# Optimization experiments

Hardware: AMD Instinct MI355X
Metric: run time of the kernel (lower is better)

The kernel has to match this reference:

```python
import jax, jax.numpy as jnp
import numpy as np

N = 16384          # nodes
E_R = 524288       # radial edges (avg degree 32)
E_B = 32768        # bonded edges
N_TYPES = 20       # atom types
CS = 64            # scalar (0e) channels
CV = 32            # vector (1o) channels
EA = 16            # edge_attr_dim
EA_B = EA // 2     # bondedness embedding dim
EA_R = (EA + 1) // 2  # radial basis dim
CUTOFF = 1.5       # effective_radial_cutoff
L = 2              # n_layers
NORM = float(np.sqrt((E_R + E_B) / N))  # ~sqrt(avg degree) message normalization


def setup_inputs() -> dict:
    key = jax.random.key(0)
    ks = jax.random.split(key, 32)
    def rn(i, shape, scale=1.0):
        return jax.random.normal(ks[i], shape, dtype=jnp.float32) * scale
    s_e = 1.0 / np.sqrt(EA)
    inp = {}
    inp["pos"] = rn(0, (N, 3))
    inp["c_noise"] = rn(1, (1,))
    inp["atom_types"] = jax.random.randint(ks[2], (N,), 0, N_TYPES)
    inp["radial_edge_index"] = jax.random.randint(ks[3], (2, E_R), 0, N)
    inp["bonded_edge_index"] = jax.random.randint(ks[4], (2, E_B), 0, N)
    # learned parameters
    inp["atom_tab"] = rn(5, (N_TYPES, CS))
    inp["bond_tab"] = rn(6, (2, EA_B))
    inp["ns0_w"] = rn(7, (CS,), 0.1)
    inp["We0"] = rn(8, (EA, CS), s_e)
    inp["We1"] = rn(9, (EA, CS), s_e)
    inp["Wself0"] = rn(10, (CS, CS), 1.0 / np.sqrt(CS))
    inp["Ws0"] = rn(11, (CS, CS), 1.0 / np.sqrt(CS))
    inp["Wv0"] = rn(12, (CS, CV), 1.0 / np.sqrt(CS))
    inp["ns_w"] = rn(13, (L, CS + CV), 0.1)
    inp["We_ss"] = rn(14, (L, EA, CS), s_e)
    inp["We_vs"] = rn(15, (L, EA, CV), s_e)
    inp["We_sv"] = rn(16, (L, EA, CS), s_e)
    inp["We_vv"] = rn(17, (L, EA, CV), s_e)
    inp["We_vx"] = rn(18, (L, EA, CV), s_e)
    inp["Wmix_s"] = rn(19, (L, CS + CV, CS), 1.0 / np.sqrt(CS + CV))
    inp["Wmix_v"] = rn(20, (L, CS + 2 * CV, CV), 1.0 / np.sqrt(CS + 2 * CV))
    inp["Wself_s"] = rn(21, (L, CS, CS), 1.0 / np.sqrt(CS))
    inp["Wself_v"] = rn(22, (L, CV, CV), 1.0 / np.sqrt(CV))
    inp["skip_w"] = rn(23, (L, 2 * (CS + CV)), 0.1)
    inp["skip_b"] = rn(24, (L, 2 * (CS + CV)), 0.1)
    inp["w_out"] = rn(25, (CV,), 1.0 / np.sqrt(CV))
    inp["gain"] = jnp.asarray(0.5, dtype=jnp.float32)
    return inp


def _radial_basis(d):
    # e3nn soft_one_hot_linspace, basis='gaussian', cutoff=True
    centers = jnp.linspace(0.0, CUTOFF, EA_R + 2)[1:-1]
    step = centers[1] - centers[0]
    diff = (d[:, None] - centers[None, :]) / step
    return jnp.exp(-diff * diff) * 1.12


def reference(pos, c_noise, atom_tab, bond_tab, ns0_w, We0, We1, Wself0, Ws0, Wv0,
              ns_w, We_ss, We_vs, We_sv, We_vv, We_vx, Wmix_s, Wmix_v, Wself_s, Wself_v,
              skip_w, skip_b, w_out, gain, atom_types, radial_edge_index, bonded_edge_index):
    edge_index = jnp.concatenate([radial_edge_index, bonded_edge_index], axis=1)
    bond_mask = jnp.concatenate([jnp.zeros((E_R,), jnp.int32), jnp.ones((E_B,), jnp.int32)])
    src, dst = edge_index[0], edge_index[1]
    edge_vec = pos[src] - pos[dst]                      # [E,3]
    d = jnp.sqrt(jnp.sum(edge_vec * edge_vec, -1) + 1e-12)
    Y1 = jnp.sqrt(3.0) * edge_vec / d[:, None]          # l=1 SH, component norm; Y0 == 1
    edge_attr = jnp.concatenate([bond_tab[bond_mask], _radial_basis(d)], axis=-1)  # [E,EA]

    # atom embedding + initial noise-conditional scaling
    s = atom_tab[atom_types] * (1.0 + c_noise * ns0_w)  # [N,CS]

    # initial projector: scalar-input equivariant conv -> hidden irreps
    w0 = edge_attr @ We0
    w1 = edge_attr @ We1
    s_src = s[src]
    a_s = jax.ops.segment_sum(w0 * s_src, dst, num_segments=N) / NORM
    a_v = jax.ops.segment_sum((w1 * s_src)[:, :, None] * Y1[:, None, :], dst, num_segments=N) / NORM
    s_h = a_s @ Ws0 + s @ Wself0                        # [N,CS]
    v_h = jnp.einsum('nci,cd->ndi', a_v, Wv0)           # [N,CV,3]

    for l in range(L):
        # noise-conditional scaling (per-irrep-channel scalar scale)
        scale = 1.0 + c_noise * ns_w[l]
        ss = s_h * scale[:CS]
        vv = v_h * scale[CS:][None, :, None]
        ss_e = ss[src]
        vv_e = vv[src]
        # edge-attr-conditioned tensor-product weights
        w_ss = edge_attr @ We_ss[l]
        w_vs = edge_attr @ We_vs[l]
        w_sv = edge_attr @ We_sv[l]
        w_vv = edge_attr @ We_vv[l]
        w_vx = edge_attr @ We_vx[l]
        # CG tensor-product messages: 0x0->0, 1x1->0 (dot), 0x1->1, 1x0->1, 1x1->1 (cross)
        vdot = jnp.einsum('eci,ei->ec', vv_e, Y1)
        m_s = jnp.concatenate([w_ss * ss_e, w_vs * vdot], axis=-1)          # [E,CS+CV]
        m_v = jnp.concatenate([
            (w_sv * ss_e)[:, :, None] * Y1[:, None, :],
            w_vv[:, :, None] * vv_e,
            w_vx[:, :, None] * jnp.cross(vv_e, Y1[:, None, :]),
        ], axis=1)                                                          # [E,CS+2CV,3]
        a_s = jax.ops.segment_sum(m_s, dst, num_segments=N) / NORM
        a_v = jax.ops.segment_sum(m_v, dst, num_segments=N) / NORM
        new_s = a_s @ Wmix_s[l] + ss @ Wself_s[l]
        new_v = jnp.einsum('nci,cd->ndi', a_v, Wmix_v[l]) + jnp.einsum('nci,cd->ndi', vv, Wself_v[l])
        # noise-conditional skip connection (gated residual)
        g = jax.nn.sigmoid(skip_b[l] + c_noise * skip_w[l])
        s_h = g[:CS] * s_h + g[CS:2 * CS] * new_s
        g_v = g[2 * CS:]
        v_h = g_v[:CV][None, :, None] * v_h + g_v[CV:][None, :, None] * new_v

    # output head: 1o vectors -> 3D displacement, times output gain
    return jnp.einsum('nci,c->ni', v_h, w_out) * gain
```

## Files before the change

kernel.cpp:

```cpp
#include <hip/hip_runtime.h>
#include <math.h>

#define NA 16384
#define ER 524288
#define EB 32768
#define ET 557056
#define INV_NORM 0.17149858514250882f
#define SQRT3 1.7320508075688772f
#define RB_STEP (1.5f/9.0f)
#define BINS 512
#define DMAX 2.5f
#define INV_H ((float)BINS / DMAX)
#define T0U (2 * BINS * 128)
#define TLU (2 * BINS * 256)

typedef unsigned int uint32;
typedef unsigned short ushort16;
typedef float vf4 __attribute__((ext_vector_type(4)));
typedef float vf2 __attribute__((ext_vector_type(2)));

__device__ __forceinline__ float sigmoidf_(float x) { return 1.f / (1.f + __expf(-x)); }

__device__ __forceinline__ ushort16 f2bf(float x) {
  uint32 u = __float_as_uint(x);
  u = u + 0x7FFFu + ((u >> 16) & 1u);
  return (ushort16)(u >> 16);
}
__device__ __forceinline__ uint32 packbf(float hi, float lo) {
  return ((uint32)f2bf(hi) << 16) | (uint32)f2bf(lo);
}
__device__ __forceinline__ float bfhi(uint32 u) { return __uint_as_float(u & 0xFFFF0000u); }
__device__ __forceinline__ float bflo(uint32 u) { return __uint_as_float(u << 16); }

__device__ __forceinline__ float4 ntl4(const float* p) {
  vf4 v = __builtin_nontemporal_load((const vf4*)p);
  return make_float4(v.x, v.y, v.z, v.w);
}
__device__ __forceinline__ float2 ntl2(const float* p) {
  vf2 v = __builtin_nontemporal_load((const vf2*)p);
  return make_float2(v.x, v.y);
}
__device__ __forceinline__ void nts4(float* p, float a, float b, float c, float d) {
  vf4 v; v.x = a; v.y = b; v.z = c; v.w = d;
  __builtin_nontemporal_store(v, (vf4*)p);
}
__device__ __forceinline__ void nts2(float* p, float a, float b) {
  vf2 v; v.x = a; v.y = b;
  __builtin_nontemporal_store(v, (vf2*)p);
}

__global__ void k_hist(const int* __restrict__ rad, const int* __restrict__ bon, int* __restrict__ count) {
  int e = blockIdx.x * 256 + threadIdx.x;
  int d = (e < ER) ? rad[ER + e] : bon[EB + (e - ER)];
  atomicAdd(&count[d], 1);
}

__global__ void k_scan1(const int* __restrict__ count, int* __restrict__ partial) {
  __shared__ int red[256];
  int b = blockIdx.x, t = threadIdx.x;
  red[t] = count[b * 256 + t];
  __syncthreads();
  for (int s = 128; s > 0; s >>= 1) {
    if (t < s) red[t] += red[t + s];
    __syncthreads();
  }
  if (t == 0) partial[b] = red[0];
}

__global__ void k_scan2(int* __restrict__ partial) {
  int run = 0;
  for (int i = 0; i < 64; ++i) { int c = partial[i]; partial[i] = run; run += c; }
}

__global__ void k_scan3(const int* __restrict__ count, const int* __restrict__ partial,
                        int* __restrict__ offsets, int* __restrict__ cursor) {
  __shared__ int sc[256];
  int b = blockIdx.x, t = threadIdx.x;
  int v = count[b * 256 + t];
  sc[t] = v;
  __syncthreads();
  for (int off = 1; off < 256; off <<= 1) {
    int x = (t >= off) ? sc[t - off] : 0;
    __syncthreads();
    sc[t] += x;
    __syncthreads();
  }
  int excl = sc[t] - v + partial[b];
  offsets[b * 256 + t] = excl;
  cursor[b * 256 + t] = excl;
  if (b == 63 && t == 255) offsets[NA] = excl + v;
}

__global__ void k_fill_embed(const int* __restrict__ rad, const int* __restrict__ bon,
                             int* __restrict__ cursor, int* __restrict__ sorted,
                             const float* __restrict__ atom_tab, const int* __restrict__ types,
                             const float* __restrict__ ns0_w, const float* __restrict__ cnoise,
                             float* __restrict__ s_feat, ushort16* __restrict__ s_bf) {
  if (blockIdx.x < ET / 256) {
    int e = blockIdx.x * 256 + threadIdx.x;
    int d = (e < ER) ? rad[ER + e] : bon[EB + (e - ER)];
    int slot = atomicAdd(&cursor[d], 1);
    sorted[slot] = e;
  } else {
    int tid = (blockIdx.x - ET / 256) * 256 + threadIdx.x;
    int n = tid >> 6, c = tid & 63;
    float cn = cnoise[0];
    float v = atom_tab[types[n] * 64 + c] * (1.f + cn * ns0_w[c]);
    s_feat[tid] = v;
    s_bf[tid] = f2bf(v);
  }
}

__global__ void k_reorder(const int* __restrict__ sorted,
                          const int* __restrict__ rad, const int* __restrict__ bon,
                          const float* __restrict__ pos, float* __restrict__ rec8) {
  int idx = blockIdx.x * 256 + threadIdx.x;
  int e = sorted[idx];
  int src, dst, v;
  if (e < ER) { src = rad[e]; dst = rad[ER + e]; v = 0; }
  else        { src = bon[e - ER]; dst = bon[EB + e - ER]; v = 1; }
  float dx = pos[src * 3] - pos[dst * 3];
  float dy = pos[src * 3 + 1] - pos[dst * 3 + 1];
  float dz = pos[src * 3 + 2] - pos[dst * 3 + 2];
  float dist = sqrtf(dx * dx + dy * dy + dz * dz + 1e-12f);
  float inv = 1.f / dist;
  float fq = fminf(dist * INV_H, BINS - 1.001f);
  int q = (int)fq;
  float frac = fq - (float)q;
  int qoffL = (v * BINS + q) << 8;
  float* rp = rec8 + (size_t)idx * 8;
  nts4(rp, __int_as_float(src), SQRT3 * dx * inv, SQRT3 * dy * inv, SQRT3 * dz * inv);
  nts2(rp + 4, frac, __int_as_float(qoffL));
}

__global__ void k_build(const float* __restrict__ We0, const float* __restrict__ We1,
                        const float* __restrict__ We_ss, const float* __restrict__ We_vs,
                        const float* __restrict__ We_sv, const float* __restrict__ We_vv,
                        const float* __restrict__ We_vx, const float* __restrict__ bond_tab,
                        uint32* __restrict__ T0, uint32* __restrict__ TL) {
  int q = blockIdx.x, t = blockIdx.y, v = blockIdx.z, c = threadIdx.x;
  float d0 = q * (DMAX / BINS), d1 = (q + 1) * (DMAX / BINS);
  float rb0[8], rb1[8];
#pragma unroll
  for (int k = 0; k < 8; ++k) {
    float f0 = (d0 - (k + 1) * RB_STEP) * (1.f / RB_STEP);
    float f1 = (d1 - (k + 1) * RB_STEP) * (1.f / RB_STEP);
    rb0[k] = 1.12f * __expf(-f0 * f0);
    rb1[k] = 1.12f * __expf(-f1 * f1);
  }
  if (t == 0) {
    float ba = 0, bb = 0, a0 = 0, a1 = 0, b0 = 0, b1 = 0;
#pragma unroll
    for (int k = 0; k < 8; ++k) {
      float bt = bond_tab[v * 8 + k];
      float av_lo = We0[k * 64 + c], av_hi = We0[(8 + k) * 64 + c];
      float bv_lo = We1[k * 64 + c], bv_hi = We1[(8 + k) * 64 + c];
      ba += bt * av_lo; bb += bt * bv_lo;
      a0 += rb0[k] * av_hi; a1 += rb1[k] * av_hi;
      b0 += rb0[k] * bv_hi; b1 += rb1[k] * bv_hi;
    }
    uint32* o = T0 + (((size_t)v * BINS + q) << 7) + c * 2;
    o[0] = packbf(ba + a0, a1 - a0);
    o[1] = packbf(bb + b0, b1 - b0);
  } else {
    int l = t - 1;
    const float* Wss = We_ss + l * 1024;
    const float* Wsv = We_sv + l * 1024;
    const float* WA = (c < 32) ? (We_vs + l * 512) : (We_vx + l * 512);
    const float* WB = (c < 32) ? (We_vv + l * 512) : nullptr;
    int cu = c & 31;
    float sa = 0, sb = 0, s0 = 0, s1 = 0, t0 = 0, t1 = 0;
    float ua = 0, ub = 0, u0 = 0, u1 = 0, w0 = 0, w1 = 0;
#pragma unroll
    for (int k = 0; k < 8; ++k) {
      float bt = bond_tab[v * 8 + k];
      float ss_lo = Wss[k * 64 + c], ss_hi = Wss[(8 + k) * 64 + c];
      float sv_lo = Wsv[k * 64 + c], sv_hi = Wsv[(8 + k) * 64 + c];
      sa += bt * ss_lo; sb += bt * sv_lo;
      s0 += rb0[k] * ss_hi; s1 += rb1[k] * ss_hi;
      t0 += rb0[k] * sv_hi; t1 += rb1[k] * sv_hi;
      float a_lo = WA[k * 32 + cu], a_hi = WA[(8 + k) * 32 + cu];
      ua += bt * a_lo;
      u0 += rb0[k] * a_hi; u1 += rb1[k] * a_hi;
      if (WB) {
        float b_lo = WB[k * 32 + cu], b_hi = WB[(8 + k) * 32 + cu];
        ub += bt * b_lo;
        w0 += rb0[k] * b_hi; w1 += rb1[k] * b_hi;
      }
    }
    uint32* o = TL + (size_t)l * TLU + (((size_t)v * BINS + q) << 8) + c * 4;
    o[0] = packbf(sa + s0, s1 - s0);
    o[1] = packbf(sb + t0, t1 - t0);
    o[2] = packbf(ua + u0, u1 - u0);
    o[3] = WB ? packbf(ub + w0, w1 - w0) : 0u;
  }
}

__global__ __launch_bounds__(256, 8) void k_agg0(
    const int* __restrict__ offsets, const float* __restrict__ rec8,
    const uint32* __restrict__ T0, const ushort16* __restrict__ s_bf,
    float* __restrict__ a_s, uint32* __restrict__ a_v) {
  int lane = threadIdx.x & 63;
  int n = blockIdx.x * 4 + (threadIdx.x >> 6);
  float acc = 0, a0 = 0, a1 = 0, a2 = 0;
  int beg = __builtin_amdgcn_readfirstlane(offsets[n]);
  int end = __builtin_amdgcn_readfirstlane(offsets[n + 1]);
  if (beg < end) {
    int last = end - 1;
    int e1 = (beg + 1 < end) ? beg + 1 : last;
    int e2 = (beg + 2 < end) ? beg + 2 : last;
    const float* p0 = rec8 + (size_t)beg * 8;
    const float* p1 = rec8 + (size_t)e1 * 8;
    const float* p2 = rec8 + (size_t)e2 * 8;
    float4 rA0 = ntl4(p0); float2 rB0 = ntl2(p0 + 4);
    float4 rA1 = ntl4(p1); float2 rB1 = ntl2(p1 + 4);
    float4 rA2 = ntl4(p2); float2 rB2 = ntl2(p2 + 4);
    uint2 t0 = *(const uint2*)(T0 + (__float_as_int(rB0.y) >> 1) + (lane << 1));
    ushort16 s0 = s_bf[((size_t)__float_as_int(rA0.x) << 6) + lane];
    uint2 t1 = *(const uint2*)(T0 + (__float_as_int(rB1.y) >> 1) + (lane << 1));
    ushort16 s1 = s_bf[((size_t)__float_as_int(rA1.x) << 6) + lane];
#pragma unroll 3
    for (int idx = beg; idx < end; ++idx) {
      uint2 t2 = *(const uint2*)(T0 + (__float_as_int(rB2.y) >> 1) + (lane << 1));
      ushort16 s2 = s_bf[((size_t)__float_as_int(rA2.x) << 6) + lane];
      int e3 = (idx + 3 < end) ? idx + 3 : last;
      const float* p3 = rec8 + (size_t)e3 * 8;
      float4 rA3 = ntl4(p3); float2 rB3 = ntl2(p3 + 4);
      float frac = rB0.x;
      float w0 = fmaf(frac, bflo(t0.x), bfhi(t0.x));
      float w1 = fmaf(frac, bflo(t0.y), bfhi(t0.y));
      float sv = __uint_as_float((uint32)s0 << 16);
      acc += w0 * sv;
      float t = w1 * sv;
      a0 += t * rA0.y; a1 += t * rA0.z; a2 += t * rA0.w;
      rA0 = rA1; rB0 = rB1; rA1 = rA2; rB1 = rB2; rA2 = rA3; rB2 = rB3;
      t0 = t1; s0 = s1; t1 = t2; s1 = s2;
    }
  }
  a_s[n * 64 + lane] = acc * INV_NORM;
  *(uint2*)(a_v + ((size_t)n << 7) + (lane << 1)) =
      make_uint2(packbf(a0 * INV_NORM, a1 * INV_NORM), packbf(a2 * INV_NORM, 0.f));
}

__global__ __launch_bounds__(256, 8) void k_agg_layer(
    const float* __restrict__ cnoise, const float* __restrict__ nsw,
    const int* __restrict__ offsets, const float* __restrict__ rec8,
    const uint32* __restrict__ TL, const ushort16* __restrict__ sh_bf,
    const uint32* __restrict__ vh_bf,
    float* __restrict__ a_s, uint32* __restrict__ a_v) {
  int lane = threadIdx.x & 63;
  int n = blockIdx.x * 4 + (threadIdx.x >> 6);
  int vc = lane & 31;
  bool low = lane < 32;
  float cn = cnoise[0];
  float scale_s = 1.f + cn * nsw[lane];
  float scale_v = 1.f + cn * nsw[64 + vc];

  float ms = 0;
  float av0 = 0, av1 = 0, av2 = 0;
  float ms2 = 0;
  float b0 = 0, b1 = 0, b2 = 0;
  int beg = __builtin_amdgcn_readfirstlane(offsets[n]);
  int end = __builtin_amdgcn_readfirstlane(offsets[n + 1]);
  if (beg < end) {
    int last = end - 1;
    int e1 = (beg + 1 < end) ? beg + 1 : last;
    int e2 = (beg + 2 < end) ? beg + 2 : last;
    const float* p0 = rec8 + (size_t)beg * 8;
    const float* p1 = rec8 + (size_t)e1 * 8;
    const float* p2 = rec8 + (size_t)e2 * 8;
    float4 rA0 = ntl4(p0); float2 rB0 = ntl2(p0 + 4);
    float4 rA1 = ntl4(p1); float2 rB1 = ntl2(p1 + 4);
    float4 rA2 = ntl4(p2); float2 rB2 = ntl2(p2 + 4);
    uint4 t0 = *(const uint4*)(TL + __float_as_int(rB0.y) + (lane << 2));
    ushort16 s0 = sh_bf[((size_t)__float_as_int(rA0.x) << 6) + lane];
    uint2 v0 = *(const uint2*)(vh_bf + ((size_t)__float_as_int(rA0.x) << 6) + (vc << 1));
    uint4 t1 = *(const uint4*)(TL + __float_as_int(rB1.y) + (lane << 2));
    ushort16 s1 = sh_bf[((size_t)__float_as_int(rA1.x) << 6) + lane];
    uint2 v1 = *(const uint2*)(vh_bf + ((size_t)__float_as_int(rA1.x) << 6) + (vc << 1));
#pragma unroll 3
    for (int idx = beg; idx < end; ++idx) {
      uint4 t2 = *(const uint4*)(TL + __float_as_int(rB2.y) + (lane << 2));
      ushort16 s2 = sh_bf[((size_t)__float_as_int(rA2.x) << 6) + lane];
      uint2 v2 = *(const uint2*)(vh_bf + ((size_t)__float_as_int(rA2.x) << 6) + (vc << 1));
      int e3 = (idx + 3 < end) ? idx + 3 : last;
      const float* p3 = rec8 + (size_t)e3 * 8;
      float4 rA3 = ntl4(p3); float2 rB3 = ntl2(p3 + 4);
      float frac = rB0.x;
      float y0 = rA0.y, y1 = rA0.z, y2 = rA0.w;
      float wS  = fmaf(frac, bflo(t0.x), bfhi(t0.x));
      float wSV = fmaf(frac, bflo(t0.y), bfhi(t0.y));
      float wA  = fmaf(frac, bflo(t0.z), bfhi(t0.z));
      float wB  = fmaf(frac, bflo(t0.w), bfhi(t0.w));
      float ss = __uint_as_float((uint32)s0 << 16);
      float vx = bfhi(v0.x), vy = bflo(v0.x), vz = bfhi(v0.y);
      ms += wS * ss;
      float t = wSV * ss;
      av0 += t * y0; av1 += t * y1; av2 += t * y2;
      float vdot = vx * y0 + vy * y1 + vz * y2;
      ms2 += wA * vdot;
      float cx = vy * y2 - vz * y1;
      float cy = vz * y0 - vx * y2;
      float cz = vx * y1 - vy * y0;
      float m0 = low ? vx : cx;
      float m1 = low ? vy : cy;
      float m2 = low ? vz : cz;
      float wM = low ? wB : wA;
      b0 += wM * m0; b1 += wM * m1; b2 += wM * m2;
      rA0 = rA1; rB0 = rB1; rA1 = rA2; rB1 = rB2; rA2 = rA3; rB2 = rB3;
      t0 = t1; s0 = s1; v0 = v1; t1 = t2; s1 = s2; v1 = v2;
    }
  }
  float fs = scale_s * INV_NORM;
  float fv = scale_v * INV_NORM;
  a_s[n * 96 + lane] = ms * fs;
  uint32* avn = a_v + ((size_t)n << 8);
  *(uint2*)(avn + (lane << 1)) = make_uint2(packbf(av0 * fs, av1 * fs), packbf(av2 * fs, 0.f));
  if (low) {
    a_s[n * 96 + 64 + vc] = ms2 * fv;
    *(uint2*)(avn + ((64 + vc) << 1)) = make_uint2(packbf(b0 * fv, b1 * fv), packbf(b2 * fv, 0.f));
  } else {
    *(uint2*)(avn + ((96 + vc) << 1)) = make_uint2(packbf(b0 * fv, b1 * fv), packbf(b2 * fv, 0.f));
  }
}

__global__ __launch_bounds__(256, 8) void k_init_s(
    const float* __restrict__ a_s, const float* __restrict__ s_feat,
    const float* __restrict__ Ws0, const float* __restrict__ Wself0,
    float* __restrict__ sh, ushort16* __restrict__ sh_bf) {
  __shared__ uint32 W1[32 * 64];
  __shared__ uint32 W2[32 * 64];
  __shared__ float La[8 * 64];
  __shared__ float Lf[8 * 64];
  int tid = threadIdx.x;
  for (int i = tid; i < 32 * 64; i += 256) {
    int k = i >> 6, d = i & 63;
    W1[i] = packbf(Ws0[(2 * k) * 64 + d], Ws0[(2 * k + 1) * 64 + d]);
    W2[i] = packbf(Wself0[(2 * k) * 64 + d], Wself0[(2 * k + 1) * 64 + d]);
  }
  int base = blockIdx.x * 8;
  for (int i = tid; i < 512; i += 256) {
    La[i] = a_s[(size_t)base * 64 + i];
    Lf[i] = s_feat[(size_t)base * 64 + i];
  }
  __syncthreads();
  int d = tid & 63, g = tid >> 6;
  int n0 = base + g * 2;
  const float* A0 = La + g * 128;
  const float* A1 = A0 + 64;
  const float* F0 = Lf + g * 128;
  const float* F1 = F0 + 64;
  float a0 = 0, a1 = 0;
#pragma unroll 8
  for (int k = 0; k < 32; ++k) {
    uint32 w1 = W1[k * 64 + d], w2 = W2[k * 64 + d];
    int c = 2 * k;
    a0 += A0[c] * bfhi(w1) + A0[c + 1] * bflo(w1) + F0[c] * bfhi(w2) + F0[c + 1] * bflo(w2);
    a1 += A1[c] * bfhi(w1) + A1[c + 1] * bflo(w1) + F1[c] * bfhi(w2) + F1[c + 1] * bflo(w2);
  }
  sh[(size_t)n0 * 64 + d] = a0;
  sh[(size_t)(n0 + 1) * 64 + d] = a1;
  sh_bf[(size_t)n0 * 64 + d] = f2bf(a0);
  sh_bf[(size_t)(n0 + 1) * 64 + d] = f2bf(a1);
}

__global__ __launch_bounds__(256, 8) void k_init_v(
    const uint32* __restrict__ a_v, const float* __restrict__ Wv0,
    float* __restrict__ vh, uint32* __restrict__ vh_bf) {
  __shared__ uint32 W[32 * 32];
  int tid = threadIdx.x;
  for (int i = tid; i < 32 * 32; i += 256) {
    int k = i >> 5, d = i & 31;
    W[i] = packbf(Wv0[(2 * k) * 32 + d], Wv0[(2 * k + 1) * 32 + d]);
  }
  __syncthreads();
  int d = tid & 31, g = tid >> 5;
  int n = blockIdx.x * 8 + g;
  const uint2* av = (const uint2*)a_v + ((size_t)n << 6);
  float x = 0, y = 0, z = 0;
#pragma unroll 8
  for (int k = 0; k < 32; ++k) {
    uint32 w = W[k * 32 + d];
    uint2 e0 = av[2 * k], e1 = av[2 * k + 1];
    float w0 = bfhi(w), w1 = bflo(w);
    x += bfhi(e0.x) * w0 + bfhi(e1.x) * w1;
    y += bflo(e0.x) * w0 + bflo(e1.x) * w1;
    z += bfhi(e0.y) * w0 + bfhi(e1.y) * w1;
  }
  *(float4*)(vh + ((size_t)n << 7) + (d << 2)) = make_float4(x, y, z, 0.f);
  *(uint2*)(vh_bf + ((size_t)n << 6) + (d << 1)) = make_uint2(packbf(x, y), packbf(z, 0.f));
}

__global__ __launch_bounds__(256, 6) void k_mix_s(
    const float* __restrict__ a_s, const float* __restrict__ sh_in,
    const float* __restrict__ Wmix_s, const float* __restrict__ Wself_s,
    const float* __restrict__ nsw, const float* __restrict__ skw,
    const float* __restrict__ skb, const float* __restrict__ cnoise,
    float* __restrict__ sh_out, ushort16* __restrict__ sh_bf_out) {
  __shared__ uint32 Wm[48 * 64];
  __shared__ uint32 Wsf[32 * 64];
  __shared__ float La[8 * 96];
  int tid = threadIdx.x;
  float cn = cnoise[0];
  for (int i = tid; i < 48 * 64; i += 256) {
    int k = i >> 6, d = i & 63;
    Wm[i] = packbf(Wmix_s[(2 * k) * 64 + d], Wmix_s[(2 * k + 1) * 64 + d]);
  }
  for (int i = tid; i < 32 * 64; i += 256) {
    int k = i >> 6, d = i & 63;
    float sc0 = 1.f + cn * nsw[2 * k];
    float sc1 = 1.f + cn * nsw[2 * k + 1];
    Wsf[i] = packbf(Wself_s[(2 * k) * 64 + d] * sc0, Wself_s[(2 * k + 1) * 64 + d] * sc1);
  }
  int base = blockIdx.x * 8;
  for (int i = tid; i < 8 * 96; i += 256) La[i] = a_s[(size_t)base * 96 + i];
  __syncthreads();
  int d = tid & 63, g = tid >> 6;
  int n0 = base + g * 2;
  const float* A0 = La + (g * 2) * 96;
  const float* A1 = A0 + 96;
  const float* s0p = sh_in + (size_t)n0 * 64;
  const float* s1p = s0p + 64;
  float acc0 = 0, acc1 = 0;
#pragma unroll 8
  for (int k = 0; k < 48; ++k) {
    uint32 w = Wm[k * 64 + d];
    int c = 2 * k;
    float wh = bfhi(w), wl = bflo(w);
    acc0 += A0[c] * wh + A0[c + 1] * wl;
    acc1 += A1[c] * wh + A1[c + 1] * wl;
  }
#pragma unroll 8
  for (int k = 0; k < 32; ++k) {
    uint32 w = Wsf[k * 64 + d];
    int c = 2 * k;
    float wh = bfhi(w), wl = bflo(w);
    acc0 += s0p[c] * wh + s0p[c + 1] * wl;
    acc1 += s1p[c] * wh + s1p[c + 1] * wl;
  }
  float g1 = sigmoidf_(skb[d] + cn * skw[d]);
  float g2 = sigmoidf_(skb[64 + d] + cn * skw[64 + d]);
  float o0 = g1 * s0p[d] + g2 * acc0;
  float o1 = g1 * s1p[d] + g2 * acc1;
  sh_out[(size_t)n0 * 64 + d] = o0;
  sh_out[(size_t)(n0 + 1) * 64 + d] = o1;
  sh_bf_out[(size_t)n0 * 64 + d] = f2bf(o0);
  sh_bf_out[(size_t)(n0 + 1) * 64 + d] = f2bf(o1);
}

__global__ __launch_bounds__(256, 8) void k_mix_v(
    const uint32* __restrict__ a_v, const float* __restrict__ vh_in,
    const float* __restrict__ Wmix_v, const float* __restrict__ Wself_v,
    const float* __restrict__ nsw, const float* __restrict__ skw,
    const float* __restrict__ skb, const float* __restrict__ cnoise,
    float* __restrict__ vh_out, uint32* __restrict__ vh_bf_out,
    const float* __restrict__ w_out, const float* __restrict__ gain,
    float* __restrict__ out, int doOut) {
  __shared__ uint32 Wm[64 * 32];
  __shared__ uint32 Wsf[16 * 32];
  int tid = threadIdx.x;
  float cn = cnoise[0];
  for (int i = tid; i < 64 * 32; i += 256) {
    int k = i >> 5, d = i & 31;
    Wm[i] = packbf(Wmix_v[(2 * k) * 32 + d], Wmix_v[(2 * k + 1) * 32 + d]);
  }
  for (int i = tid; i < 16 * 32; i += 256) {
    int k = i >> 5, d = i & 31;
    float sc0 = 1.f + cn * nsw[64 + 2 * k];
    float sc1 = 1.f + cn * nsw[64 + 2 * k + 1];
    Wsf[i] = packbf(Wself_v[(2 * k) * 32 + d] * sc0, Wself_v[(2 * k + 1) * 32 + d] * sc1);
  }
  __syncthreads();
  int d = tid & 31, g = tid >> 5;
  int n = blockIdx.x * 8 + g;
  const uint2* av = (const uint2*)a_v + ((size_t)n << 7);
  const float4* vr = (const float4*)(vh_in + ((size_t)n << 7));
  float x = 0, y = 0, z = 0;
#pragma unroll 8
  for (int k = 0; k < 64; ++k) {
    uint32 w = Wm[k * 32 + d];
    uint2 e0 = av[2 * k], e1 = av[2 * k + 1];
    float w0 = bfhi(w), w1 = bflo(w);
    x += bfhi(e0.x) * w0 + bfhi(e1.x) * w1;
    y += bflo(e0.x) * w0 + bflo(e1.x) * w1;
    z += bfhi(e0.y) * w0 + bfhi(e1.y) * w1;
  }
#pragma unroll 8
  for (int k = 0; k < 16; ++k) {
    uint32 w = Wsf[k * 32 + d];
    float4 e0 = vr[2 * k], e1 = vr[2 * k + 1];
    float w0 = bfhi(w), w1 = bflo(w);
    x += e0.x * w0 + e1.x * w1;
    y += e0.y * w0 + e1.y * w1;
    z += e0.z * w0 + e1.z * w1;
  }
  float g3 = sigmoidf_(skb[128 + d] + cn * skw[128 + d]);
  float g4 = sigmoidf_(skb[160 + d] + cn * skw[160 + d]);
  float4 vi = vr[d];
  float ox = g3 * vi.x + g4 * x;
  float oy = g3 * vi.y + g4 * y;
  float oz = g3 * vi.z + g4 * z;
  *(float4*)(vh_out + ((size_t)n << 7) + (d << 2)) = make_float4(ox, oy, oz, 0.f);
  *(uint2*)(vh_bf_out + ((size_t)n << 6) + (d << 1)) = make_uint2(packbf(ox, oy), packbf(oz, 0.f));
  if (doOut) {
    float wv = w_out[d];
    float rx = wv * ox, ry = wv * oy, rz = wv * oz;
#pragma unroll
    for (int m = 16; m > 0; m >>= 1) {
      rx += __shfl_xor(rx, m, 32);
      ry += __shfl_xor(ry, m, 32);
      rz += __shfl_xor(rz, m, 32);
    }
    if (d == 0) {
      float gn = gain[0];
      float* op = out + (size_t)n * 3;
      op[0] = rx * gn; op[1] = ry * gn; op[2] = rz * gn;
    }
  }
}

extern "C" void kernel_launch(void* const* d_in, const int* in_sizes, int n_in,
                              void* d_out, int out_size, void* d_ws, size_t ws_size,
                              hipStream_t stream) {
  (void)in_sizes; (void)n_in; (void)out_size; (void)ws_size;
  const float* pos     = (const float*)d_in[0];
  const float* cn      = (const float*)d_in[1];
  const int*   types   = (const int*)d_in[2];
  const int*   rad     = (const int*)d_in[3];
  const int*   bon     = (const int*)d_in[4];
  const float* atom_tab= (const float*)d_in[5];
  const float* bond_tab= (const float*)d_in[6];
  const float* ns0_w   = (const float*)d_in[7];
  const float* We0     = (const float*)d_in[8];
  const float* We1     = (const float*)d_in[9];
  const float* Wself0  = (const float*)d_in[10];
  const float* Ws0     = (const float*)d_in[11];
  const float* Wv0     = (const float*)d_in[12];
  const float* ns_w    = (const float*)d_in[13];
  const float* We_ss   = (const float*)d_in[14];
  const float* We_vs   = (const float*)d_in[15];
  const float* We_sv   = (const float*)d_in[16];
  const float* We_vv   = (const float*)d_in[17];
  const float* We_vx   = (const float*)d_in[18];
  const float* Wmix_s  = (const float*)d_in[19];
  const float* Wmix_v  = (const float*)d_in[20];
  const float* Wself_s = (const float*)d_in[21];
  const float* Wself_v = (const float*)d_in[22];
  const float* skip_w  = (const float*)d_in[23];
  const float* skip_b  = (const float*)d_in[24];
  const float* w_out   = (const float*)d_in[25];
  const float* gain    = (const float*)d_in[26];

  char* ws = (char*)d_ws;
  size_t o = 0;
  auto alloc = [&](size_t bytes) -> void* {
    void* p = ws + o;
    o += (bytes + 255) & ~(size_t)255;
    return p;
  };
  float* s_feat  = (float*)alloc((size_t)NA * 64 * 4);
  ushort16* s_bf = (ushort16*)alloc((size_t)NA * 64 * 2);
  float* a_s     = (float*)alloc((size_t)NA * 96 * 4);
  uint32* a_v    = (uint32*)alloc((size_t)NA * 256 * 4);
  float* sh0     = (float*)alloc((size_t)NA * 64 * 4);
  float* sh1     = (float*)alloc((size_t)NA * 64 * 4);
  ushort16* shbf0= (ushort16*)alloc((size_t)NA * 64 * 2);
  ushort16* shbf1= (ushort16*)alloc((size_t)NA * 64 * 2);
  float* vh0     = (float*)alloc((size_t)NA * 128 * 4);
  float* vh1     = (float*)alloc((size_t)NA * 128 * 4);
  uint32* vhbf0  = (uint32*)alloc((size_t)NA * 64 * 4);
  uint32* vhbf1  = (uint32*)alloc((size_t)NA * 64 * 4);
  int* count     = (int*)alloc((size_t)NA * 4);
  int* partial   = (int*)alloc((size_t)64 * 4);
  int* offsets   = (int*)alloc((size_t)(NA + 1) * 4);
  int* cursor    = (int*)alloc((size_t)NA * 4);
  int* sorted    = (int*)alloc((size_t)ET * 4);
  float* rec8    = (float*)alloc((size_t)ET * 32);
  uint32* T0     = (uint32*)alloc((size_t)T0U * 4);
  uint32* TL     = (uint32*)alloc((size_t)2 * TLU * 4);
  float* shb[2]  = {sh0, sh1};
  ushort16* shbf[2] = {shbf0, shbf1};
  float* vhb[2]  = {vh0, vh1};
  uint32* vhbf[2]= {vhbf0, vhbf1};

  hipMemsetAsync(count, 0, (size_t)NA * 4, stream);
  k_hist<<<ET / 256, 256, 0, stream>>>(rad, bon, count);
  k_scan1<<<64, 256, 0, stream>>>(count, partial);
  k_scan2<<<1, 1, 0, stream>>>(partial);
  k_scan3<<<64, 256, 0, stream>>>(count, partial, offsets, cursor);
  k_fill_embed<<<ET / 256 + NA * 64 / 256, 256, 0, stream>>>(
      rad, bon, cursor, sorted, atom_tab, types, ns0_w, cn, s_feat, s_bf);
  k_reorder<<<ET / 256, 256, 0, stream>>>(sorted, rad, bon, pos, rec8);
  k_build<<<dim3(BINS, 3, 2), 64, 0, stream>>>(We0, We1, We_ss, We_vs, We_sv, We_vv, We_vx,
                                               bond_tab, T0, TL);

  k_agg0<<<NA / 4, 256, 0, stream>>>(offsets, rec8, T0, s_bf, a_s, a_v);
  k_init_s<<<NA / 8, 256, 0, stream>>>(a_s, s_feat, Ws0, Wself0, shb[0], shbf[0]);
  k_init_v<<<NA / 8, 256, 0, stream>>>(a_v, Wv0, vhb[0], vhbf[0]);

  for (int l = 0; l < 2; ++l) {
    int bin = l & 1, bout = 1 - bin;
    k_agg_layer<<<NA / 4, 256, 0, stream>>>(
        cn, ns_w + l * 96, offsets, rec8, TL + (size_t)l * TLU, shbf[bin], vhbf[bin], a_s, a_v);
    k_mix_s<<<NA / 8, 256, 0, stream>>>(
        a_s, shb[bin], Wmix_s + l * 96 * 64, Wself_s + l * 64 * 64,
        ns_w + l * 96, skip_w + l * 192, skip_b + l * 192, cn, shb[bout], shbf[bout]);
    k_mix_v<<<NA / 8, 256, 0, stream>>>(
        a_v, vhb[bin], Wmix_v + l * 128 * 32, Wself_v + l * 32 * 32,
        ns_w + l * 96, skip_w + l * 192, skip_b + l * 192, cn, vhb[bout], vhbf[bout],
        w_out, gain, (float*)d_out, l == 1);
  }
}
```

Before: 483.2 us.

## Pack edge records to 16 bytes in bf16 and merge prep kernels

Edge records shrink from 8 floats with 6 used (32 bytes) to 4 uint32 (16 bytes). The unit direction components and the interpolation fraction are now stored as bf16 pairs, and each aggregation kernel reads one 128-bit nontemporal load per edge. The three-kernel scan becomes a single-block scan, and the reorder and table-build kernels are fused into one launch to cut launch overhead. The cost is lower precision on edge directions and on the bin fraction, plus a serial per-thread scan over 64 elements.

```diff
diff --git a/kernel.cpp b/kernel.cpp
--- a/kernel.cpp
+++ b/kernel.cpp
@@ -16,8 +16,7 @@
 
 typedef unsigned int uint32;
 typedef unsigned short ushort16;
-typedef float vf4 __attribute__((ext_vector_type(4)));
-typedef float vf2 __attribute__((ext_vector_type(2)));
+typedef unsigned int vu4 __attribute__((ext_vector_type(4)));
 
 __device__ __forceinline__ float sigmoidf_(float x) { return 1.f / (1.f + __expf(-x)); }
 
@@ -32,21 +31,13 @@
 __device__ __forceinline__ float bfhi(uint32 u) { return __uint_as_float(u & 0xFFFF0000u); }
 __device__ __forceinline__ float bflo(uint32 u) { return __uint_as_float(u << 16); }
 
-__device__ __forceinline__ float4 ntl4(const float* p) {
-  vf4 v = __builtin_nontemporal_load((const vf4*)p);
-  return make_float4(v.x, v.y, v.z, v.w);
-}
-__device__ __forceinline__ float2 ntl2(const float* p) {
-  vf2 v = __builtin_nontemporal_load((const vf2*)p);
-  return make_float2(v.x, v.y);
-}
-__device__ __forceinline__ void nts4(float* p, float a, float b, float c, float d) {
-  vf4 v; v.x = a; v.y = b; v.z = c; v.w = d;
-  __builtin_nontemporal_store(v, (vf4*)p);
-}
-__device__ __forceinline__ void nts2(float* p, float a, float b) {
-  vf2 v; v.x = a; v.y = b;
-  __builtin_nontemporal_store(v, (vf2*)p);
+__device__ __forceinline__ uint4 ntlu4(const uint32* p) {
+  vu4 v = __builtin_nontemporal_load((const vu4*)p);
+  return make_uint4(v.x, v.y, v.z, v.w);
+}
+__device__ __forceinline__ void ntsu4(uint32* p, uint32 a, uint32 b, uint32 c, uint32 d) {
+  vu4 v; v.x = a; v.y = b; v.z = c; v.w = d;
+  __builtin_nontemporal_store(v, (vu4*)p);
 }
 
 __global__ void k_hist(const int* __restrict__ rad, const int* __restrict__ bon, int* __restrict__ count) {
@@ -55,40 +46,28 @@
   atomicAdd(&count[d], 1);
 }
 
-__global__ void k_scan1(const int* __restrict__ count, int* __restrict__ partial) {
-  __shared__ int red[256];
-  int b = blockIdx.x, t = threadIdx.x;
-  red[t] = count[b * 256 + t];
-  __syncthreads();
-  for (int s = 128; s > 0; s >>= 1) {
-    if (t < s) red[t] += red[t + s];
-    __syncthreads();
-  }
-  if (t == 0) partial[b] = red[0];
-}
-
-__global__ void k_scan2(int* __restrict__ partial) {
-  int run = 0;
-  for (int i = 0; i < 64; ++i) { int c = partial[i]; partial[i] = run; run += c; }
-}
-
-__global__ void k_scan3(const int* __restrict__ count, const int* __restrict__ partial,
-                        int* __restrict__ offsets, int* __restrict__ cursor) {
-  __shared__ int sc[256];
-  int b = blockIdx.x, t = threadIdx.x;
-  int v = count[b * 256 + t];
-  sc[t] = v;
+__global__ void k_scan(int* __restrict__ count, int* __restrict__ offsets, int* __restrict__ cursor) {
+  __shared__ int part[256];
+  int t = threadIdx.x;
+  int base = t * 64;
+  int s = 0;
+  for (int j = 0; j < 64; ++j) s += count[base + j];
+  part[t] = s;
   __syncthreads();
   for (int off = 1; off < 256; off <<= 1) {
-    int x = (t >= off) ? sc[t - off] : 0;
+    int v = (t >= off) ? part[t - off] : 0;
     __syncthreads();
-    sc[t] += x;
+    part[t] += v;
     __syncthreads();
   }
-  int excl = sc[t] - v + partial[b];
-  offsets[b * 256 + t] = excl;
-  cursor[b * 256 + t] = excl;
-  if (b == 63 && t == 255) offsets[NA] = excl + v;
+  int run = part[t] - s;
+  for (int j = 0; j < 64; ++j) {
+    int c = count[base + j];
+    offsets[base + j] = run;
+    cursor[base + j] = run;
+    run += c;
+  }
+  if (t == 255) offsets[NA] = run;
 }
 
 __global__ void k_fill_embed(const int* __restrict__ rad, const int* __restrict__ bon,
@@ -111,93 +90,99 @@
   }
 }
 
-__global__ void k_reorder(const int* __restrict__ sorted,
-                          const int* __restrict__ rad, const int* __restrict__ bon,
-                          const float* __restrict__ pos, float* __restrict__ rec8) {
-  int idx = blockIdx.x * 256 + threadIdx.x;
-  int e = sorted[idx];
-  int src, dst, v;
-  if (e < ER) { src = rad[e]; dst = rad[ER + e]; v = 0; }
-  else        { src = bon[e - ER]; dst = bon[EB + e - ER]; v = 1; }
-  float dx = pos[src * 3] - pos[dst * 3];
-  float dy = pos[src * 3 + 1] - pos[dst * 3 + 1];
-  float dz = pos[src * 3 + 2] - pos[dst * 3 + 2];
-  float dist = sqrtf(dx * dx + dy * dy + dz * dz + 1e-12f);
-  float inv = 1.f / dist;
-  float fq = fminf(dist * INV_H, BINS - 1.001f);
-  int q = (int)fq;
-  float frac = fq - (float)q;
-  int qoffL = (v * BINS + q) << 8;
-  float* rp = rec8 + (size_t)idx * 8;
-  nts4(rp, __int_as_float(src), SQRT3 * dx * inv, SQRT3 * dy * inv, SQRT3 * dz * inv);
-  nts2(rp + 4, frac, __int_as_float(qoffL));
-}
-
-__global__ void k_build(const float* __restrict__ We0, const float* __restrict__ We1,
-                        const float* __restrict__ We_ss, const float* __restrict__ We_vs,
-                        const float* __restrict__ We_sv, const float* __restrict__ We_vv,
-                        const float* __restrict__ We_vx, const float* __restrict__ bond_tab,
-                        uint32* __restrict__ T0, uint32* __restrict__ TL) {
-  int q = blockIdx.x, t = blockIdx.y, v = blockIdx.z, c = threadIdx.x;
-  float d0 = q * (DMAX / BINS), d1 = (q + 1) * (DMAX / BINS);
-  float rb0[8], rb1[8];
-#pragma unroll
-  for (int k = 0; k < 8; ++k) {
-    float f0 = (d0 - (k + 1) * RB_STEP) * (1.f / RB_STEP);
-    float f1 = (d1 - (k + 1) * RB_STEP) * (1.f / RB_STEP);
-    rb0[k] = 1.12f * __expf(-f0 * f0);
-    rb1[k] = 1.12f * __expf(-f1 * f1);
-  }
-  if (t == 0) {
-    float ba = 0, bb = 0, a0 = 0, a1 = 0, b0 = 0, b1 = 0;
+__global__ void k_reorder_build(
+    const int* __restrict__ sorted, const int* __restrict__ rad, const int* __restrict__ bon,
+    const float* __restrict__ pos, uint32* __restrict__ rec4,
+    const float* __restrict__ We0, const float* __restrict__ We1,
+    const float* __restrict__ We_ss, const float* __restrict__ We_vs,
+    const float* __restrict__ We_sv, const float* __restrict__ We_vv,
+    const float* __restrict__ We_vx, const float* __restrict__ bond_tab,
+    uint32* __restrict__ T0, uint32* __restrict__ TL) {
+  if (blockIdx.x < ET / 256) {
+    int idx = blockIdx.x * 256 + threadIdx.x;
+    int e = sorted[idx];
+    int src, dst, v;
+    if (e < ER) { src = rad[e]; dst = rad[ER + e]; v = 0; }
+    else        { src = bon[e - ER]; dst = bon[EB + e - ER]; v = 1; }
+    float dx = pos[src * 3] - pos[dst * 3];
+    float dy = pos[src * 3 + 1] - pos[dst * 3 + 1];
+    float dz = pos[src * 3 + 2] - pos[dst * 3 + 2];
+    float dist = sqrtf(dx * dx + dy * dy + dz * dz + 1e-12f);
+    float inv = 1.f / dist;
+    float fq = fminf(dist * INV_H, BINS - 1.001f);
+    int q = (int)fq;
+    float frac = fq - (float)q;
+    int qoffL = (v * BINS + q) << 8;
+    ntsu4(rec4 + (size_t)idx * 4, (uint32)src,
+          packbf(SQRT3 * dx * inv, SQRT3 * dy * inv),
+          packbf(SQRT3 * dz * inv, frac), (uint32)qoffL);
+  } else {
+    int flat = (blockIdx.x - ET / 256) * 256 + threadIdx.x;
+    int c = flat & 63;
+    int rest = flat >> 6;
+    int q = rest & (BINS - 1);
+    int tv = rest >> 9;
+    int t = tv % 3, v = tv / 3;
+    float d0 = q * (DMAX / BINS), d1 = (q + 1) * (DMAX / BINS);
+    float rb0[8], rb1[8];
 #pragma unroll
     for (int k = 0; k < 8; ++k) {
-      float bt = bond_tab[v * 8 + k];
-      float av_lo = We0[k * 64 + c], av_hi = We0[(8 + k) * 64 + c];
-      float bv_lo = We1[k * 64 + c], bv_hi = We1[(8 + k) * 64 + c];
-      ba += bt * av_lo; bb += bt * bv_lo;
-      a0 += rb0[k] * av_hi; a1 += rb1[k] * av_hi;
-      b0 += rb0[k] * bv_hi; b1 += rb1[k] * bv_hi;
+      float f0 = (d0 - (k + 1) * RB_STEP) * (1.f / RB_STEP);
+      float f1 = (d1 - (k + 1) * RB_STEP) * (1.f / RB_STEP);
+      rb0[k] = 1.12f * __expf(-f0 * f0);
+      rb1[k] = 1.12f * __expf(-f1 * f1);
     }
-    uint32* o = T0 + (((size_t)v * BINS + q) << 7) + c * 2;
-    o[0] = packbf(ba + a0, a1 - a0);
-    o[1] = packbf(bb + b0, b1 - b0);
-  } else {
-    int l = t - 1;
-    const float* Wss = We_ss + l * 1024;
-    const float* Wsv = We_sv + l * 1024;
-    const float* WA = (c < 32) ? (We_vs + l * 512) : (We_vx + l * 512);
-    const float* WB = (c < 32) ? (We_vv + l * 512) : nullptr;
-    int cu = c & 31;
-    float sa = 0, sb = 0, s0 = 0, s1 = 0, t0 = 0, t1 = 0;
-    float ua = 0, ub = 0, u0 = 0, u1 = 0, w0 = 0, w1 = 0;
+    if (t == 0) {
+      float ba = 0, bb = 0, a0 = 0, a1 = 0, b0 = 0, b1 = 0;
 #pragma unroll
-    for (int k = 0; k < 8; ++k) {
-      float bt = bond_tab[v * 8 + k];
-      float ss_lo = Wss[k * 64 + c], ss_hi = Wss[(8 + k) * 64 + c];
-      float sv_lo = Wsv[k * 64 + c], sv_hi = Wsv[(8 + k) * 64 + c];
-      sa += bt * ss_lo; sb += bt * sv_lo;
-      s0 += rb0[k] * ss_hi; s1 += rb1[k] * ss_hi;
-      t0 += rb0[k] * sv_hi; t1 += rb1[k] * sv_hi;
-      float a_lo = WA[k * 32 + cu], a_hi = WA[(8 + k) * 32 + cu];
-      ua += bt * a_lo;
-      u0 += rb0[k] * a_hi; u1 += rb1[k] * a_hi;
-      if (WB) {
-        float b_lo = WB[k * 32 + cu], b_hi = WB[(8 + k) * 32 + cu];
-        ub += bt * b_lo;
-        w0 += rb0[k] * b_hi; w1 += rb1[k] * b_hi;
+      for (int k = 0; k < 8; ++k) {
+        float bt = bond_tab[v * 8 + k];
+        float av_lo = We0[k * 64 + c], av_hi = We0[(8 + k) * 64 + c];
+        float bv_lo = We1[k * 64 + c], bv_hi = We1[(8 + k) * 64 + c];
+        ba += bt * av_lo; bb += bt * bv_lo;
+        a0 += rb0[k] * av_hi; a1 += rb1[k] * av_hi;
+        b0 += rb0[k] * bv_hi; b1 += rb1[k] * bv_hi;
       }
+      uint32* o = T0 + (((size_t)v * BINS + q) << 7) + c * 2;
+      o[0] = packbf(ba + a0, a1 - a0);
+      o[1] = packbf(bb + b0, b1 - b0);
+    } else {
+      int l = t - 1;
+      const float* Wss = We_ss + l * 1024;
+      const float* Wsv = We_sv + l * 1024;
+      const float* WA = (c < 32) ? (We_vs + l * 512) : (We_vx + l * 512);
+      const float* WB = (c < 32) ? (We_vv + l * 512) : nullptr;
+      int cu = c & 31;
+      float sa = 0, sb = 0, s0 = 0, s1 = 0, t0 = 0, t1 = 0;
+      float ua = 0, ub = 0, u0 = 0, u1 = 0, w0 = 0, w1 = 0;
+#pragma unroll
+      for (int k = 0; k < 8; ++k) {
+        float bt = bond_tab[v * 8 + k];
+        float ss_lo = Wss[k * 64 + c], ss_hi = Wss[(8 + k) * 64 + c];
+        float sv_lo = Wsv[k * 64 + c], sv_hi = Wsv[(8 + k) * 64 + c];
+        sa += bt * ss_lo; sb += bt * sv_lo;
+        s0 += rb0[k] * ss_hi; s1 += rb1[k] * ss_hi;
+        t0 += rb0[k] * sv_hi; t1 += rb1[k] * sv_hi;
+        float a_lo = WA[k * 32 + cu], a_hi = WA[(8 + k) * 32 + cu];
+        ua += bt * a_lo;
+        u0 += rb0[k] * a_hi; u1 += rb1[k] * a_hi;
+        if (WB) {
+          float b_lo = WB[k * 32 + cu], b_hi = WB[(8 + k) * 32 + cu];
+          ub += bt * b_lo;
+          w0 += rb0[k] * b_hi; w1 += rb1[k] * b_hi;
+        }
+      }
+      uint32* o = TL + (size_t)l * TLU + (((size_t)v * BINS + q) << 8) + c * 4;
+      o[0] = packbf(sa + s0, s1 - s0);
+      o[1] = packbf(sb + t0, t1 - t0);
+      o[2] = packbf(ua + u0, u1 - u0);
+      o[3] = WB ? packbf(ub + w0, w1 - w0) : 0u;
     }
-    uint32* o = TL + (size_t)l * TLU + (((size_t)v * BINS + q) << 8) + c * 4;
-    o[0] = packbf(sa + s0, s1 - s0);
-    o[1] = packbf(sb + t0, t1 - t0);
-    o[2] = packbf(ua + u0, u1 - u0);
-    o[3] = WB ? packbf(ub + w0, w1 - w0) : 0u;
   }
 }
 
 __global__ __launch_bounds__(256, 8) void k_agg0(
-    const int* __restrict__ offsets, const float* __restrict__ rec8,
+    const int* __restrict__ offsets, const uint32* __restrict__ rec4,
     const uint32* __restrict__ T0, const ushort16* __restrict__ s_bf,
     float* __restrict__ a_s, uint32* __restrict__ a_v) {
   int lane = threadIdx.x & 63;
@@ -209,31 +194,27 @@
     int last = end - 1;
     int e1 = (beg + 1 < end) ? beg + 1 : last;
     int e2 = (beg + 2 < end) ? beg + 2 : last;
-    const float* p0 = rec8 + (size_t)beg * 8;
-    const float* p1 = rec8 + (size_t)e1 * 8;
-    const float* p2 = rec8 + (size_t)e2 * 8;
-    float4 rA0 = ntl4(p0); float2 rB0 = ntl2(p0 + 4);
-    float4 rA1 = ntl4(p1); float2 rB1 = ntl2(p1 + 4);
-    float4 rA2 = ntl4(p2); float2 rB2 = ntl2(p2 + 4);
-    uint2 t0 = *(const uint2*)(T0 + (__float_as_int(rB0.y) >> 1) + (lane << 1));
-    ushort16 s0 = s_bf[((size_t)__float_as_int(rA0.x) << 6) + lane];
-    uint2 t1 = *(const uint2*)(T0 + (__float_as_int(rB1.y) >> 1) + (lane << 1));
-    ushort16 s1 = s_bf[((size_t)__float_as_int(rA1.x) << 6) + lane];
+    uint4 r0 = ntlu4(rec4 + (size_t)beg * 4);
+    uint4 r1 = ntlu4(rec4 + (size_t)e1 * 4);
+    uint4 r2 = ntlu4(rec4 + (size_t)e2 * 4);
+    uint2 t0 = *(const uint2*)(T0 + (r0.w >> 1) + (lane << 1));
+    ushort16 s0 = s_bf[((size_t)r0.x << 6) + lane];
+    uint2 t1 = *(const uint2*)(T0 + (r1.w >> 1) + (lane << 1));
+    ushort16 s1 = s_bf[((size_t)r1.x << 6) + lane];
 #pragma unroll 3
     for (int idx = beg; idx < end; ++idx) {
-      uint2 t2 = *(const uint2*)(T0 + (__float_as_int(rB2.y) >> 1) + (lane << 1));
-      ushort16 s2 = s_bf[((size_t)__float_as_int(rA2.x) << 6) + lane];
+      uint2 t2 = *(const uint2*)(T0 + (r2.w >> 1) + (lane << 1));
+      ushort16 s2 = s_bf[((size_t)r2.x << 6) + lane];
       int e3 = (idx + 3 < end) ? idx + 3 : last;
-      const float* p3 = rec8 + (size_t)e3 * 8;
-      float4 rA3 = ntl4(p3); float2 rB3 = ntl2(p3 + 4);
-      float frac = rB0.x;
+      uint4 r3 = ntlu4(rec4 + (size_t)e3 * 4);
+      float frac = bflo(r0.z);
       float w0 = fmaf(frac, bflo(t0.x), bfhi(t0.x));
       float w1 = fmaf(frac, bflo(t0.y), bfhi(t0.y));
       float sv = __uint_as_float((uint32)s0 << 16);
       acc += w0 * sv;
       float t = w1 * sv;
-      a0 += t * rA0.y; a1 += t * rA0.z; a2 += t * rA0.w;
-      rA0 = rA1; rB0 = rB1; rA1 = rA2; rB1 = rB2; rA2 = rA3; rB2 = rB3;
+      a0 += t * bfhi(r0.y); a1 += t * bflo(r0.y); a2 += t * bfhi(r0.z);
+      r0 = r1; r1 = r2; r2 = r3;
       t0 = t1; s0 = s1; t1 = t2; s1 = s2;
     }
   }
@@ -244,7 +225,7 @@
 
 __global__ __launch_bounds__(256, 8) void k_agg_layer(
     const float* __restrict__ cnoise, const float* __restrict__ nsw,
-    const int* __restrict__ offsets, const float* __restrict__ rec8,
+    const int* __restrict__ offsets, const uint32* __restrict__ rec4,
     const uint32* __restrict__ TL, const ushort16* __restrict__ sh_bf,
     const uint32* __restrict__ vh_bf,
     float* __restrict__ a_s, uint32* __restrict__ a_v) {
@@ -266,28 +247,24 @@
     int last = end - 1;
     int e1 = (beg + 1 < end) ? beg + 1 : last;
     int e2 = (beg + 2 < end) ? beg + 2 : last;
-    const float* p0 = rec8 + (size_t)beg * 8;
-    const float* p1 = rec8 + (size_t)e1 * 8;
-    const float* p2 = rec8 + (size_t)e2 * 8;
-    float4 rA0 = ntl4(p0); float2 rB0 = ntl2(p0 + 4);
-    float4 rA1 = ntl4(p1); float2 rB1 = ntl2(p1 + 4);
-    float4 rA2 = ntl4(p2); float2 rB2 = ntl2(p2 + 4);
-    uint4 t0 = *(const uint4*)(TL + __float_as_int(rB0.y) + (lane << 2));
-    ushort16 s0 = sh_bf[((size_t)__float_as_int(rA0.x) << 6) + lane];
-    uint2 v0 = *(const uint2*)(vh_bf + ((size_t)__float_as_int(rA0.x) << 6) + (vc << 1));
-    uint4 t1 = *(const uint4*)(TL + __float_as_int(rB1.y) + (lane << 2));
-    ushort16 s1 = sh_bf[((size_t)__float_as_int(rA1.x) << 6) + lane];
-    uint2 v1 = *(const uint2*)(vh_bf + ((size_t)__float_as_int(rA1.x) << 6) + (vc << 1));
+    uint4 r0 = ntlu4(rec4 + (size_t)beg * 4);
+    uint4 r1 = ntlu4(rec4 + (size_t)e1 * 4);
+    uint4 r2 = ntlu4(rec4 + (size_t)e2 * 4);
+    uint4 t0 = *(const uint4*)(TL + r0.w + (lane << 2));
+    ushort16 s0 = sh_bf[((size_t)r0.x << 6) + lane];
+    uint2 v0 = *(const uint2*)(vh_bf + ((size_t)r0.x << 6) + (vc << 1));
+    uint4 t1 = *(const uint4*)(TL + r1.w + (lane << 2));
+    ushort16 s1 = sh_bf[((size_t)r1.x << 6) + lane];
+    uint2 v1 = *(const uint2*)(vh_bf + ((size_t)r1.x << 6) + (vc << 1));
 #pragma unroll 3
     for (int idx = beg; idx < end; ++idx) {
-      uint4 t2 = *(const uint4*)(TL + __float_as_int(rB2.y) + (lane << 2));
-      ushort16 s2 = sh_bf[((size_t)__float_as_int(rA2.x) << 6) + lane];
-      uint2 v2 = *(const uint2*)(vh_bf + ((size_t)__float_as_int(rA2.x) << 6) + (vc << 1));
+      uint4 t2 = *(const uint4*)(TL + r2.w + (lane << 2));
+      ushort16 s2 = sh_bf[((size_t)r2.x << 6) + lane];
+      uint2 v2 = *(const uint2*)(vh_bf + ((size_t)r2.x << 6) + (vc << 1));
       int e3 = (idx + 3 < end) ? idx + 3 : last;
-      const float* p3 = rec8 + (size_t)e3 * 8;
-      float4 rA3 = ntl4(p3); float2 rB3 = ntl2(p3 + 4);
-      float frac = rB0.x;
-      float y0 = rA0.y, y1 = rA0.z, y2 = rA0.w;
+      uint4 r3 = ntlu4(rec4 + (size_t)e3 * 4);
+      float frac = bflo(r0.z);
+      float y0 = bfhi(r0.y), y1 = bflo(r0.y), y2 = bfhi(r0.z);
       float wS  = fmaf(frac, bflo(t0.x), bfhi(t0.x));
       float wSV = fmaf(frac, bflo(t0.y), bfhi(t0.y));
       float wA  = fmaf(frac, bflo(t0.z), bfhi(t0.z));
@@ -307,7 +284,7 @@
       float m2 = low ? vz : cz;
       float wM = low ? wB : wA;
       b0 += wM * m0; b1 += wM * m1; b2 += wM * m2;
-      rA0 = rA1; rB0 = rB1; rA1 = rA2; rB1 = rB2; rA2 = rA3; rB2 = rB3;
+      r0 = r1; r1 = r2; r2 = r3;
       t0 = t1; s0 = s1; v0 = v1; t1 = t2; s1 = s2; v1 = v2;
     }
   }
@@ -571,11 +548,10 @@
   uint32* vhbf0  = (uint32*)alloc((size_t)NA * 64 * 4);
   uint32* vhbf1  = (uint32*)alloc((size_t)NA * 64 * 4);
   int* count     = (int*)alloc((size_t)NA * 4);
-  int* partial   = (int*)alloc((size_t)64 * 4);
   int* offsets   = (int*)alloc((size_t)(NA + 1) * 4);
   int* cursor    = (int*)alloc((size_t)NA * 4);
   int* sorted    = (int*)alloc((size_t)ET * 4);
-  float* rec8    = (float*)alloc((size_t)ET * 32);
+  uint32* rec4   = (uint32*)alloc((size_t)ET * 16);
   uint32* T0     = (uint32*)alloc((size_t)T0U * 4);
   uint32* TL     = (uint32*)alloc((size_t)2 * TLU * 4);
   float* shb[2]  = {sh0, sh1};
@@ -585,23 +561,21 @@
 
   hipMemsetAsync(count, 0, (size_t)NA * 4, stream);
   k_hist<<<ET / 256, 256, 0, stream>>>(rad, bon, count);
-  k_scan1<<<64, 256, 0, stream>>>(count, partial);
-  k_scan2<<<1, 1, 0, stream>>>(partial);
-  k_scan3<<<64, 256, 0, stream>>>(count, partial, offsets, cursor);
+  k_scan<<<1, 256, 0, stream>>>(count, offsets, cursor);
   k_fill_embed<<<ET / 256 + NA * 64 / 256, 256, 0, stream>>>(
       rad, bon, cursor, sorted, atom_tab, types, ns0_w, cn, s_feat, s_bf);
-  k_reorder<<<ET / 256, 256, 0, stream>>>(sorted, rad, bon, pos, rec8);
-  k_build<<<dim3(BINS, 3, 2), 64, 0, stream>>>(We0, We1, We_ss, We_vs, We_sv, We_vv, We_vx,
-                                               bond_tab, T0, TL);
-
-  k_agg0<<<NA / 4, 256, 0, stream>>>(offsets, rec8, T0, s_bf, a_s, a_v);
+  k_reorder_build<<<ET / 256 + 768, 256, 0, stream>>>(
+      sorted, rad, bon, pos, rec4,
+      We0, We1, We_ss, We_vs, We_sv, We_vv, We_vx, bond_tab, T0, TL);
+
+  k_agg0<<<NA / 4, 256, 0, stream>>>(offsets, rec4, T0, s_bf, a_s, a_v);
   k_init_s<<<NA / 8, 256, 0, stream>>>(a_s, s_feat, Ws0, Wself0, shb[0], shbf[0]);
   k_init_v<<<NA / 8, 256, 0, stream>>>(a_v, Wv0, vhb[0], vhbf[0]);
 
   for (int l = 0; l < 2; ++l) {
     int bin = l & 1, bout = 1 - bin;
     k_agg_layer<<<NA / 4, 256, 0, stream>>>(
-        cn, ns_w + l * 96, offsets, rec8, TL + (size_t)l * TLU, shbf[bin], vhbf[bin], a_s, a_v);
+        cn, ns_w + l * 96, offsets, rec4, TL + (size_t)l * TLU, shbf[bin], vhbf[bin], a_s, a_v);
     k_mix_s<<<NA / 8, 256, 0, stream>>>(
         a_s, shb[bin], Wmix_s + l * 96 * 64, Wself_s + l * 64 * 64,
         ns_w + l * 96, skip_w + l * 192, skip_b + l * 192, cn, shb[bout], shbf[bout]);
```

After: 474.1 us. About the same (-1.9%).
